# Kernel tuning notes

Hardware: AMD Instinct MI355X
Metric: run time of the kernel (lower is better)

## Reference

```python
import jax, jax.numpy as jnp
import numpy as np

DIM = 512
HEADS = 8
DIM_HEAD = 64
INNER = HEADS * DIM_HEAD  # 512
EPS = 1e-5


def setup_inputs() -> dict:
    key = jax.random.key(0)
    ks = jax.random.split(key, 8)
    b, n = 4, 2048
    x = jax.random.normal(ks[0], (b, n, DIM), dtype=jnp.float32)
    ln_g = jnp.ones((DIM,), jnp.float32)
    ln_b = jnp.zeros((DIM,), jnp.float32)
    w_qkv = jax.random.normal(ks[1], (DIM, 3 * INNER), jnp.float32) * (DIM ** -0.5)
    reattn_w = jax.random.normal(ks[2], (HEADS, HEADS), jnp.float32)
    rn_g = jnp.ones((HEADS,), jnp.float32)
    rn_b = jnp.zeros((HEADS,), jnp.float32)
    w_out = jax.random.normal(ks[3], (INNER, DIM), jnp.float32) * (INNER ** -0.5)
    b_out = jnp.zeros((DIM,), jnp.float32)
    return {"x": x, "ln_g": ln_g, "ln_b": ln_b, "w_qkv": w_qkv,
            "reattn_w": reattn_w, "rn_g": rn_g, "rn_b": rn_b,
            "w_out": w_out, "b_out": b_out}


def _layernorm(x, g, b, axis=-1):
    mu = jnp.mean(x, axis=axis, keepdims=True)
    var = jnp.var(x, axis=axis, keepdims=True)
    return (x - mu) * jax.lax.rsqrt(var + EPS) * g + b


def reference(x, ln_g, ln_b, w_qkv, reattn_w, rn_g, rn_b, w_out, b_out):
    b, n, _ = x.shape
    h, d = HEADS, DIM_HEAD
    scale = d ** -0.5
    xn = _layernorm(x, ln_g, ln_b)                       # [b,n,dim]
    qkv = xn @ w_qkv                                     # [b,n,3*inner]
    q, k, v = jnp.split(qkv, 3, axis=-1)
    to_heads = lambda t: t.reshape(b, n, h, d).transpose(0, 2, 1, 3)  # [b,h,n,d]
    q, k, v = to_heads(q), to_heads(k), to_heads(v)
    dots = jnp.einsum('bhid,bhjd->bhij', q, k) * scale   # [b,h,n,n]
    attn = jax.nn.softmax(dots, axis=-1)
    # cross-head re-attention mixing
    attn = jnp.einsum('bhij,hg->bgij', attn, reattn_w)
    # LayerNorm over the head axis (axis=1), affine params shaped [h]
    attn = _layernorm(attn, rn_g[None, :, None, None], rn_b[None, :, None, None], axis=1)
    out = jnp.einsum('bhij,bhjd->bhid', attn, v)         # [b,h,n,d]
    out = out.transpose(0, 2, 1, 3).reshape(b, n, h * d)
    return out @ w_out + b_out
```

## Files before the change

### kernel.cpp

```cpp
#include <hip/hip_runtime.h>
#include <hip/hip_bf16.h>
#include <math.h>

#define DEV __device__ __forceinline__

typedef short bf16x8 __attribute__((ext_vector_type(8)));
typedef short bf16x4 __attribute__((ext_vector_type(4)));
typedef float f32x4 __attribute__((ext_vector_type(4)));

static const int Nn = 2048;
static const int DIMd = 512;

DEV float bf2f(short u) {
    union { unsigned int i; float f; } c;
    c.i = ((unsigned int)(unsigned short)u) << 16;
    return c.f;
}

DEV short f2bf(float f) {
    union { float f; unsigned int i; } c;
    c.f = f;
    unsigned int u = c.i;
    unsigned int r = (u + 0x7fffu + ((u >> 16) & 1u)) >> 16;
    return (short)r;
}

DEV void gload16(const short* __restrict__ g, short* l) {
    __builtin_amdgcn_global_load_lds(
        (__attribute__((address_space(1))) void*)g,
        (__attribute__((address_space(3))) void*)l, 16, 0, 0);
}

__global__ void k_transpose_cast(const float* __restrict__ src,
                                 short* __restrict__ dst, int K, int N) {
    int o = blockIdx.x * 256 + threadIdx.x;
    if (o >= K * N) return;
    int n = o / K, k = o - n * K;
    dst[o] = f2bf(src[(size_t)k * N + n]);
}

__global__ __launch_bounds__(256) void k_ln(const float* __restrict__ x,
                                            const float* __restrict__ g,
                                            const float* __restrict__ bta,
                                            short* __restrict__ xn) {
    int row = blockIdx.x * 4 + (threadIdx.x >> 6);
    int lane = threadIdx.x & 63;
    const float* xr = x + (size_t)row * DIMd;
    float4 v0 = ((const float4*)xr)[lane * 2];
    float4 v1 = ((const float4*)xr)[lane * 2 + 1];
    float f[8] = {v0.x, v0.y, v0.z, v0.w, v1.x, v1.y, v1.z, v1.w};
    float s = 0.f, sq = 0.f;
#pragma unroll
    for (int t = 0; t < 8; ++t) { s += f[t]; sq += f[t] * f[t]; }
#pragma unroll
    for (int off = 32; off >= 1; off >>= 1) {
        s += __shfl_xor(s, off);
        sq += __shfl_xor(sq, off);
    }
    float mu = s * (1.0f / 512.0f);
    float var = sq * (1.0f / 512.0f) - mu * mu;
    float rs = rsqrtf(var + 1e-5f);
    bf16x8 o;
#pragma unroll
    for (int t = 0; t < 8; ++t) {
        int c = lane * 8 + t;
        o[t] = f2bf((f[t] - mu) * rs * g[c] + bta[c]);
    }
    *(bf16x8*)(xn + (size_t)row * DIMd + lane * 8) = o;
}

DEV void gemm128_loop(const short* __restrict__ A, const short* __restrict__ B,
                      int K, int i0, int n0, int tid,
                      short* As, short* Bs, f32x4 acc[4][4]) {
    const int w = tid >> 6, wr = w >> 1, wc = w & 1;
    const int lane = tid & 63, fr = lane & 15, fq = lane >> 4;
    const int sr = tid >> 3, sc = (tid & 7) * 8;
    for (int k0 = 0; k0 < K; k0 += 64) {
#pragma unroll
        for (int L = 0; L < 4; ++L) {
            gload16(A + (size_t)(i0 + L * 32 + sr) * K + k0 + sc,
                    As + (L * 32 + sr) * 64 + sc);
            gload16(B + (size_t)(n0 + L * 32 + sr) * K + k0 + sc,
                    Bs + (L * 32 + sr) * 64 + sc);
        }
        __syncthreads();
#pragma unroll
        for (int kk = 0; kk < 2; ++kk) {
            bf16x8 af[4], bfr[4];
#pragma unroll
            for (int m = 0; m < 4; ++m)
                af[m] = *(const bf16x8*)(As + (wr * 64 + m * 16 + fr) * 64 + kk * 32 + fq * 8);
#pragma unroll
            for (int n = 0; n < 4; ++n)
                bfr[n] = *(const bf16x8*)(Bs + (wc * 64 + n * 16 + fr) * 64 + kk * 32 + fq * 8);
#pragma unroll
            for (int m = 0; m < 4; ++m)
#pragma unroll
                for (int n = 0; n < 4; ++n)
                    acc[m][n] = __builtin_amdgcn_mfma_f32_16x16x32_bf16(af[m], bfr[n], acc[m][n], 0, 0, 0);
        }
        __syncthreads();
    }
}

__global__ __launch_bounds__(256) void k_qkv(const short* __restrict__ xn,
                                             const short* __restrict__ wT,
                                             short* __restrict__ Q,
                                             short* __restrict__ Kb,
                                             short* __restrict__ Vt) {
    __shared__ short As[128 * 64], Bs[128 * 64];
    int tid = threadIdx.x;
    int i0 = blockIdx.x * 128, n0 = blockIdx.y * 128;
    f32x4 acc[4][4] = {};
    gemm128_loop(xn, wT, DIMd, i0, n0, tid, As, Bs, acc);
    const int w = tid >> 6, wr = w >> 1, wc = w & 1;
    const int lane = tid & 63, fr = lane & 15, fq = lane >> 4;
#pragma unroll
    for (int m = 0; m < 4; ++m) {
#pragma unroll
        for (int n = 0; n < 4; ++n) {
#pragma unroll
            for (int r = 0; r < 4; ++r) {
                int row = i0 + wr * 64 + m * 16 + fq * 4 + r;
                int c = n0 + wc * 64 + n * 16 + fr;
                short hv = f2bf(acc[m][n][r]);
                int b = row >> 11, i = row & 2047;
                int t = c >> 9, rem = c & 511;
                int h = rem >> 6, dd = rem & 63;
                size_t bh = (size_t)(b * 8 + h);
                if (t == 0)      Q [(bh * Nn + i) * 64 + dd] = hv;
                else if (t == 1) Kb[(bh * Nn + i) * 64 + dd] = hv;
                else             Vt[(bh * 64 + dd) * Nn + i] = hv;
            }
        }
    }
}

__global__ __launch_bounds__(256) void k_out(const short* __restrict__ outh,
                                             const short* __restrict__ wT,
                                             const float* __restrict__ bias,
                                             float* __restrict__ out) {
    __shared__ short As[128 * 64], Bs[128 * 64];
    int tid = threadIdx.x;
    int i0 = blockIdx.x * 128, n0 = blockIdx.y * 128;
    f32x4 acc[4][4] = {};
    gemm128_loop(outh, wT, 512, i0, n0, tid, As, Bs, acc);
    const int w = tid >> 6, wr = w >> 1, wc = w & 1;
    const int lane = tid & 63, fr = lane & 15, fq = lane >> 4;
#pragma unroll
    for (int m = 0; m < 4; ++m)
#pragma unroll
        for (int n = 0; n < 4; ++n)
#pragma unroll
            for (int r = 0; r < 4; ++r) {
                int row = i0 + wr * 64 + m * 16 + fq * 4 + r;
                int c = n0 + wc * 64 + n * 16 + fr;
                out[(size_t)row * 512 + c] = acc[m][n][r] + bias[c];
            }
}

DEV void decode_bid(int bid, int& b, int& i0) {
    int xcd = bid & 7, slot = bid >> 3;
    b = xcd >> 1;
    i0 = ((xcd & 1) * 32 + slot) * 32;
}

__global__ __launch_bounds__(512) void k_stats(const short* __restrict__ Q,
                                               const short* __restrict__ Kb,
                                               float* __restrict__ zstat) {
    int b, i0;
    decode_bid(blockIdx.x, b, i0);
    int tid = threadIdx.x, wv = tid >> 6, lane = tid & 63;
    int fr = lane & 15, fq = lane >> 4;
    size_t bh = (size_t)(b * 8 + wv);
    const short* qb = Q + (bh * Nn + i0) * 64;
    bf16x8 qf[2][2];
#pragma unroll
    for (int in = 0; in < 2; ++in)
#pragma unroll
        for (int kk = 0; kk < 2; ++kk)
            qf[in][kk] = *(const bf16x8*)(qb + (in * 16 + fr) * 64 + kk * 32 + fq * 8);
    float m[2] = {-1e30f, -1e30f}, l[2] = {0.f, 0.f};
    const short* kbase = Kb + bh * Nn * 64;
    for (int jt = 0; jt < 32; ++jt) {
        const short* kb = kbase + jt * 64 * 64;
        f32x4 acc[4][2] = {};
#pragma unroll
        for (int kk = 0; kk < 2; ++kk)
#pragma unroll
            for (int jm = 0; jm < 4; ++jm) {
                bf16x8 kf = *(const bf16x8*)(kb + (jm * 16 + fr) * 64 + kk * 32 + fq * 8);
                acc[jm][0] = __builtin_amdgcn_mfma_f32_16x16x32_bf16(kf, qf[0][kk], acc[jm][0], 0, 0, 0);
                acc[jm][1] = __builtin_amdgcn_mfma_f32_16x16x32_bf16(kf, qf[1][kk], acc[jm][1], 0, 0, 0);
            }
#pragma unroll
        for (int in = 0; in < 2; ++in) {
            float mt = acc[0][in][0];
#pragma unroll
            for (int jm = 0; jm < 4; ++jm)
#pragma unroll
                for (int r = 0; r < 4; ++r) mt = fmaxf(mt, acc[jm][in][r]);
            mt = fmaxf(mt, __shfl_xor(mt, 16));
            mt = fmaxf(mt, __shfl_xor(mt, 32));
            float es = 0.f;
#pragma unroll
            for (int jm = 0; jm < 4; ++jm)
#pragma unroll
                for (int r = 0; r < 4; ++r)
                    es += __expf((acc[jm][in][r] - mt) * 0.125f);
            es += __shfl_xor(es, 16);
            es += __shfl_xor(es, 32);
            float mn = fmaxf(m[in], mt);
            l[in] = l[in] * __expf((m[in] - mn) * 0.125f) + es * __expf((mt - mn) * 0.125f);
            m[in] = mn;
        }
    }
    if (fq == 0) {
#pragma unroll
        for (int in = 0; in < 2; ++in)
            zstat[bh * Nn + i0 + in * 16 + fr] = m[in] * 0.125f + __logf(l[in]);
    }
}

__global__ __launch_bounds__(512)
__attribute__((amdgpu_waves_per_eu(2, 2)))
void k_fused(const short* __restrict__ Q, const short* __restrict__ Kb,
             const short* __restrict__ Vt, const float* __restrict__ zstat,
             const float* __restrict__ R, const float* __restrict__ rg,
             const float* __restrict__ rb, short* __restrict__ outh) {
    __shared__ short S_lds[8 * 32 * 64];
    __shared__ short P_lds[8 * 32 * 64];
    __shared__ float Rraw[64], Rc[64], rgs[8], rbs[8], zl[8 * 32];
    int b, i0;
    decode_bid(blockIdx.x, b, i0);
    int tid = threadIdx.x, wv = tid >> 6, lane = tid & 63;
    int fr = lane & 15, fq = lane >> 4;
    if (tid < 64) Rraw[tid] = R[tid];
    if (tid < 8) { rgs[tid] = rg[tid]; rbs[tid] = rb[tid]; }
    if (tid >= 64 && tid < 320) {
        int q = tid - 64;
        zl[q] = zstat[(size_t)(b * 8 + (q >> 5)) * Nn + i0 + (q & 31)];
    }
    __syncthreads();
    if (tid < 64) {
        int h = tid >> 3;
        float mn = 0.f;
#pragma unroll
        for (int gg = 0; gg < 8; ++gg) mn += Rraw[h * 8 + gg];
        Rc[tid] = Rraw[tid] - mn * 0.125f;
    }
    size_t bh = (size_t)(b * 8 + wv);
    const short* qb = Q + (bh * Nn + i0) * 64;
    bf16x8 qf[2][2];
#pragma unroll
    for (int in = 0; in < 2; ++in)
#pragma unroll
        for (int kk = 0; kk < 2; ++kk)
            qf[in][kk] = *(const bf16x8*)(qb + (in * 16 + fr) * 64 + kk * 32 + fq * 8);
    float zh[2] = {zl[wv * 32 + fr], zl[wv * 32 + 16 + fr]};
    const short* kbase = Kb + bh * Nn * 64;
    const short* vbase = Vt + bh * 64 * Nn;
    const int mi = tid >> 4, j4 = (tid & 15) * 4;
    const int msw = (mi & 7) << 4;
    f32x4 acc_o[2][4] = {};
    for (int jt = 0; jt < 32; ++jt) {
        {
            const short* kb = kbase + jt * 64 * 64;
            f32x4 acc[4][2] = {};
#pragma unroll
            for (int kk = 0; kk < 2; ++kk)
#pragma unroll
                for (int jm = 0; jm < 4; ++jm) {
                    bf16x8 kf = *(const bf16x8*)(kb + (jm * 16 + fr) * 64 + kk * 32 + fq * 8);
                    acc[jm][0] = __builtin_amdgcn_mfma_f32_16x16x32_bf16(kf, qf[0][kk], acc[jm][0], 0, 0, 0);
                    acc[jm][1] = __builtin_amdgcn_mfma_f32_16x16x32_bf16(kf, qf[1][kk], acc[jm][1], 0, 0, 0);
                }
#pragma unroll
            for (int in = 0; in < 2; ++in) {
                int i = in * 16 + fr;
                int sw = (i & 7) << 4;
#pragma unroll
                for (int jm = 0; jm < 4; ++jm) {
                    bf16x4 pk;
#pragma unroll
                    for (int r = 0; r < 4; ++r)
                        pk[r] = f2bf(__expf(acc[jm][in][r] * 0.125f - zh[in]));
                    int j0 = jm * 16 + fq * 4;
                    *(bf16x4*)((char*)S_lds + wv * 4096 + i * 128 + ((j0 * 2) ^ sw)) = pk;
                }
            }
        }
        __syncthreads();
        {
            bf16x4 sh[8];
#pragma unroll
            for (int h = 0; h < 8; ++h)
                sh[h] = *(const bf16x4*)((char*)S_lds + h * 4096 + mi * 128 + ((j4 * 2) ^ msw));
            bf16x4 og[8];
#pragma unroll
            for (int e = 0; e < 4; ++e) {
                float pv[8];
#pragma unroll
                for (int h = 0; h < 8; ++h) pv[h] = bf2f(sh[h][e]);
                float cc[8];
#pragma unroll
                for (int gg = 0; gg < 8; ++gg) {
                    float s = 0.f;
#pragma unroll
                    for (int h = 0; h < 8; ++h) s += pv[h] * Rc[h * 8 + gg];
                    cc[gg] = s;
                }
                float var = 0.f;
#pragma unroll
                for (int gg = 0; gg < 8; ++gg) var += cc[gg] * cc[gg];
                var *= 0.125f;
                float rs_ = rsqrtf(var + 1e-5f);
#pragma unroll
                for (int gg = 0; gg < 8; ++gg)
                    og[gg][e] = f2bf(cc[gg] * rs_ * rgs[gg] + rbs[gg]);
            }
#pragma unroll
            for (int gg = 0; gg < 8; ++gg)
                *(bf16x4*)((char*)P_lds + gg * 4096 + mi * 128 + ((j4 * 2) ^ msw)) = og[gg];
        }
        __syncthreads();
        {
            const short* vb = vbase + jt * 64;
#pragma unroll
            for (int kk = 0; kk < 2; ++kk) {
                bf16x8 vf[4];
#pragma unroll
                for (int dn = 0; dn < 4; ++dn)
                    vf[dn] = *(const bf16x8*)(vb + (size_t)(dn * 16 + fr) * Nn + kk * 32 + fq * 8);
#pragma unroll
                for (int im = 0; im < 2; ++im) {
                    int row = im * 16 + fr;
                    bf16x8 pa = *(const bf16x8*)((char*)P_lds + wv * 4096 + row * 128 +
                                                 (((kk * 32 + fq * 8) * 2) ^ ((row & 7) << 4)));
#pragma unroll
                    for (int dn = 0; dn < 4; ++dn)
                        acc_o[im][dn] = __builtin_amdgcn_mfma_f32_16x16x32_bf16(pa, vf[dn], acc_o[im][dn], 0, 0, 0);
                }
            }
        }
        __syncthreads();
    }
#pragma unroll
    for (int im = 0; im < 2; ++im)
#pragma unroll
        for (int dn = 0; dn < 4; ++dn)
#pragma unroll
            for (int r = 0; r < 4; ++r)
                outh[((size_t)b * Nn + i0 + im * 16 + fq * 4 + r) * 512 + wv * 64 + dn * 16 + fr] =
                    f2bf(acc_o[im][dn][r]);
}

extern "C" void kernel_launch(void* const* d_in, const int* in_sizes, int n_in,
                              void* d_out, int out_size, void* d_ws, size_t ws_size,
                              hipStream_t stream) {
    const float* x      = (const float*)d_in[0];
    const float* ln_g   = (const float*)d_in[1];
    const float* ln_b   = (const float*)d_in[2];
    const float* w_qkv  = (const float*)d_in[3];
    const float* reattn = (const float*)d_in[4];
    const float* rn_g   = (const float*)d_in[5];
    const float* rn_b   = (const float*)d_in[6];
    const float* w_out  = (const float*)d_in[7];
    const float* b_out  = (const float*)d_in[8];
    float* out = (float*)d_out;

    char* ws = (char*)d_ws;
    short* wqkvT = (short*)ws; ws += (size_t)1536 * 512 * 2;
    short* woutT = (short*)ws; ws += (size_t)512 * 512 * 2;
    short* xn    = (short*)ws; ws += (size_t)8192 * 512 * 2;
    short* Q     = (short*)ws; ws += (size_t)32 * 2048 * 64 * 2;
    short* Kb    = (short*)ws; ws += (size_t)32 * 2048 * 64 * 2;
    short* Vt    = (short*)ws; ws += (size_t)32 * 64 * 2048 * 2;
    short* outh  = (short*)ws; ws += (size_t)8192 * 512 * 2;
    float* zstat = (float*)xn;

    k_transpose_cast<<<(512 * 1536 + 255) / 256, 256, 0, stream>>>(w_qkv, wqkvT, 512, 1536);
    k_transpose_cast<<<(512 * 512 + 255) / 256, 256, 0, stream>>>(w_out, woutT, 512, 512);
    k_ln<<<8192 / 4, 256, 0, stream>>>(x, ln_g, ln_b, xn);
    k_qkv<<<dim3(8192 / 128, 1536 / 128), 256, 0, stream>>>(xn, wqkvT, Q, Kb, Vt);

    k_stats<<<256, 512, 0, stream>>>(Q, Kb, zstat);
    k_fused<<<256, 512, 0, stream>>>(Q, Kb, Vt, zstat, reattn, rn_g, rn_b, outh);

    k_out<<<dim3(8192 / 128, 512 / 128), 256, 0, stream>>>(outh, woutT, b_out, out);
}
```

Measured before the change: 352.8 us.

## Split attention key range in two halves across blocks with combine kernels

The stats and fused attention kernels now split the key dimension in half, doubling the grid from 256 to 512 blocks. Partial softmax max/sum statistics are merged in a new k_zcomb kernel, and partial fp32 outputs are summed and cast to bf16 in a new k_osum kernel. The aim is to fill more compute units on the GPU, since 256 blocks underuse the device. The cost is two extra launches and a 32 MB fp32 partial-output round trip through memory. Launch bounds also change from a fixed two waves per EU to min-blocks 4.

Result: faster. 341.9 us (-3.1%).

```diff
diff --git a/kernel.cpp b/kernel.cpp
--- a/kernel.cpp
+++ b/kernel.cpp
@@ -159,17 +159,19 @@
             }
 }
 
-DEV void decode_bid(int bid, int& b, int& i0) {
+DEV void decode_bid2(int bid, int& b, int& i0, int& jh) {
     int xcd = bid & 7, slot = bid >> 3;
     b = xcd >> 1;
-    i0 = ((xcd & 1) * 32 + slot) * 32;
-}
-
-__global__ __launch_bounds__(512) void k_stats(const short* __restrict__ Q,
-                                               const short* __restrict__ Kb,
-                                               float* __restrict__ zstat) {
-    int b, i0;
-    decode_bid(blockIdx.x, b, i0);
+    jh = xcd & 1;
+    i0 = slot * 32;
+}
+
+__global__ __launch_bounds__(512, 4) void k_stats(const short* __restrict__ Q,
+                                                  const short* __restrict__ Kb,
+                                                  float* __restrict__ mpart,
+                                                  float* __restrict__ lpart) {
+    int b, i0, jh;
+    decode_bid2(blockIdx.x, b, i0, jh);
     int tid = threadIdx.x, wv = tid >> 6, lane = tid & 63;
     int fr = lane & 15, fq = lane >> 4;
     size_t bh = (size_t)(b * 8 + wv);
@@ -181,8 +183,8 @@
         for (int kk = 0; kk < 2; ++kk)
             qf[in][kk] = *(const bf16x8*)(qb + (in * 16 + fr) * 64 + kk * 32 + fq * 8);
     float m[2] = {-1e30f, -1e30f}, l[2] = {0.f, 0.f};
-    const short* kbase = Kb + bh * Nn * 64;
-    for (int jt = 0; jt < 32; ++jt) {
+    const short* kbase = Kb + bh * Nn * 64 + (size_t)jh * 1024 * 64;
+    for (int jt = 0; jt < 16; ++jt) {
         const short* kb = kbase + jt * 64 * 64;
         f32x4 acc[4][2] = {};
 #pragma unroll
@@ -217,22 +219,35 @@
     }
     if (fq == 0) {
 #pragma unroll
-        for (int in = 0; in < 2; ++in)
-            zstat[bh * Nn + i0 + in * 16 + fr] = m[in] * 0.125f + __logf(l[in]);
-    }
-}
-
-__global__ __launch_bounds__(512)
-__attribute__((amdgpu_waves_per_eu(2, 2)))
+        for (int in = 0; in < 2; ++in) {
+            size_t o = (size_t)jh * 65536 + bh * Nn + i0 + in * 16 + fr;
+            mpart[o] = m[in];
+            lpart[o] = l[in];
+        }
+    }
+}
+
+__global__ __launch_bounds__(256) void k_zcomb(const float* __restrict__ mpart,
+                                               const float* __restrict__ lpart,
+                                               float* __restrict__ zstat) {
+    int idx = blockIdx.x * 256 + threadIdx.x;
+    float m0 = mpart[idx], m1 = mpart[65536 + idx];
+    float l0 = lpart[idx], l1 = lpart[65536 + idx];
+    float M = fmaxf(m0, m1);
+    float L = l0 * __expf((m0 - M) * 0.125f) + l1 * __expf((m1 - M) * 0.125f);
+    zstat[idx] = M * 0.125f + __logf(L);
+}
+
+__global__ __launch_bounds__(512, 4)
 void k_fused(const short* __restrict__ Q, const short* __restrict__ Kb,
              const short* __restrict__ Vt, const float* __restrict__ zstat,
              const float* __restrict__ R, const float* __restrict__ rg,
-             const float* __restrict__ rb, short* __restrict__ outh) {
+             const float* __restrict__ rb, float* __restrict__ opart) {
     __shared__ short S_lds[8 * 32 * 64];
     __shared__ short P_lds[8 * 32 * 64];
     __shared__ float Rraw[64], Rc[64], rgs[8], rbs[8], zl[8 * 32];
-    int b, i0;
-    decode_bid(blockIdx.x, b, i0);
+    int b, i0, jh;
+    decode_bid2(blockIdx.x, b, i0, jh);
     int tid = threadIdx.x, wv = tid >> 6, lane = tid & 63;
     int fr = lane & 15, fq = lane >> 4;
     if (tid < 64) Rraw[tid] = R[tid];
@@ -258,12 +273,12 @@
         for (int kk = 0; kk < 2; ++kk)
             qf[in][kk] = *(const bf16x8*)(qb + (in * 16 + fr) * 64 + kk * 32 + fq * 8);
     float zh[2] = {zl[wv * 32 + fr], zl[wv * 32 + 16 + fr]};
-    const short* kbase = Kb + bh * Nn * 64;
-    const short* vbase = Vt + bh * 64 * Nn;
+    const short* kbase = Kb + bh * Nn * 64 + (size_t)jh * 1024 * 64;
+    const short* vbase = Vt + bh * 64 * Nn + (size_t)jh * 1024;
     const int mi = tid >> 4, j4 = (tid & 15) * 4;
     const int msw = (mi & 7) << 4;
     f32x4 acc_o[2][4] = {};
-    for (int jt = 0; jt < 32; ++jt) {
+    for (int jt = 0; jt < 16; ++jt) {
         {
             const short* kb = kbase + jt * 64 * 64;
             f32x4 acc[4][2] = {};
@@ -345,14 +360,25 @@
         }
         __syncthreads();
     }
+    float* po = opart + (size_t)jh * 4194304 + ((size_t)b * Nn + i0) * 512;
 #pragma unroll
     for (int im = 0; im < 2; ++im)
 #pragma unroll
         for (int dn = 0; dn < 4; ++dn)
 #pragma unroll
             for (int r = 0; r < 4; ++r)
-                outh[((size_t)b * Nn + i0 + im * 16 + fq * 4 + r) * 512 + wv * 64 + dn * 16 + fr] =
-                    f2bf(acc_o[im][dn][r]);
+                po[(im * 16 + fq * 4 + r) * 512 + wv * 64 + dn * 16 + fr] = acc_o[im][dn][r];
+}
+
+__global__ __launch_bounds__(256) void k_osum(const float* __restrict__ opart,
+                                              short* __restrict__ outh) {
+    int base = (blockIdx.x * 256 + threadIdx.x) * 4;
+    f32x4 a = *(const f32x4*)(opart + base);
+    f32x4 c = *(const f32x4*)(opart + 4194304 + base);
+    bf16x4 o;
+#pragma unroll
+    for (int t = 0; t < 4; ++t) o[t] = f2bf(a[t] + c[t]);
+    *(bf16x4*)(outh + base) = o;
 }
 
 extern "C" void kernel_launch(void* const* d_in, const int* in_sizes, int n_in,
@@ -377,6 +403,9 @@
     short* Kb    = (short*)ws; ws += (size_t)32 * 2048 * 64 * 2;
     short* Vt    = (short*)ws; ws += (size_t)32 * 64 * 2048 * 2;
     short* outh  = (short*)ws; ws += (size_t)8192 * 512 * 2;
+    float* opart = (float*)ws; ws += (size_t)2 * 4194304 * 4;
+    float* mpart = (float*)ws; ws += (size_t)2 * 65536 * 4;
+    float* lpart = (float*)ws; ws += (size_t)2 * 65536 * 4;
     float* zstat = (float*)xn;
 
     k_transpose_cast<<<(512 * 1536 + 255) / 256, 256, 0, stream>>>(w_qkv, wqkvT, 512, 1536);
@@ -384,8 +413,10 @@
     k_ln<<<8192 / 4, 256, 0, stream>>>(x, ln_g, ln_b, xn);
     k_qkv<<<dim3(8192 / 128, 1536 / 128), 256, 0, stream>>>(xn, wqkvT, Q, Kb, Vt);
 
-    k_stats<<<256, 512, 0, stream>>>(Q, Kb, zstat);
-    k_fused<<<256, 512, 0, stream>>>(Q, Kb, Vt, zstat, reattn, rn_g, rn_b, outh);
+    k_stats<<<512, 512, 0, stream>>>(Q, Kb, mpart, lpart);
+    k_zcomb<<<256, 256, 0, stream>>>(mpart, lpart, zstat);
+    k_fused<<<512, 512, 0, stream>>>(Q, Kb, Vt, zstat, reattn, rn_g, rn_b, opart);
+    k_osum<<<4096, 256, 0, stream>>>(opart, outh);
 
     k_out<<<dim3(8192 / 128, 512 / 128), 256, 0, stream>>>(outh, woutT, b_out, out);
 }
```
